# Kernel tuning notes

Hardware: AMD Instinct MI355X
Metric: run time of the kernel (lower is better)

Reference implementation:

```python
import jax, jax.numpy as jnp
import numpy as np


def setup_inputs() -> dict:
    key = jax.random.key(0)
    ks = jax.random.split(key, 7)
    B, C, N, F = 4, 8, 2048, 64
    H, O = 64, 64
    s_in = 1.0 / np.sqrt(F)
    s_h = 1.0 / np.sqrt(H)
    return {
        "x": jax.random.normal(ks[0], (B, C, N, F), dtype=jnp.float32),
        "W1": jax.random.uniform(ks[1], (H, F), jnp.float32, -s_in, s_in),
        "b1": jax.random.uniform(ks[2], (H,), jnp.float32, -s_in, s_in),
        "W2": jax.random.uniform(ks[3], (H, F), jnp.float32, -s_in, s_in),
        "b2": jax.random.uniform(ks[4], (H,), jnp.float32, -s_in, s_in),
        "W3": jax.random.uniform(ks[5], (O, F), jnp.float32, -s_in, s_in),
        "b3": jax.random.uniform(ks[6], (O,), jnp.float32, -s_in, s_in),
    }


def reference(x, W1, b1, W2, b2, W3, b3):
    # e1, e2: [B,C,N,H]  (torch Linear: x @ W^T + b)
    e1 = jnp.einsum("bcnf,hf->bcnh", x, W1) + b1
    e2 = jnp.einsum("bcnf,hf->bcnh", x, W2) + b2
    # adjacency via ReLU(e1 @ e2^T): [B,C,N,N]
    adj = jax.nn.relu(jnp.einsum("bcnh,bcmh->bcnm", e1, e2))
    # propagate: [B,C,N,F]
    h = jnp.einsum("bcnm,bcmf->bcnf", adj, x)
    # output projection (linear3): [B,C,N,O]
    return jnp.einsum("bcnf,of->bcno", h, W3) + b3
```

## Files before the change

### kernel.cpp

```cpp
#include <hip/hip_runtime.h>
#include <hip/hip_bf16.h>

#define BCH 32
#define NN  2048
#define DD  64

typedef __attribute__((ext_vector_type(8)))  __bf16 bf16x8;
typedef __attribute__((ext_vector_type(4)))  __bf16 bf16x4;
typedef __attribute__((ext_vector_type(4)))  float  f32x4;
typedef __attribute__((ext_vector_type(16))) float  f32x16;
typedef __attribute__((ext_vector_type(2)))  int    i32x2;
typedef __attribute__((ext_vector_type(4)))  int    i32x4;
typedef __attribute__((ext_vector_type(2)))  unsigned int u32x2;

__device__ inline f32x4 mfma16(bf16x8 a, bf16x8 b, f32x4 c) {
    return __builtin_amdgcn_mfma_f32_16x16x32_bf16(a, b, c, 0, 0, 0);
}
__device__ inline f32x16 mfma32(bf16x8 a, bf16x8 b, f32x16 c) {
    return __builtin_amdgcn_mfma_f32_32x32x16_bf16(a, b, c, 0, 0, 0);
}
__device__ inline void gload16(const void* g, void* l) {
    __builtin_amdgcn_global_load_lds(
        (const __attribute__((address_space(1))) void*)g,
        (__attribute__((address_space(3))) void*)l, 16, 0, 0);
}
__device__ inline void plswap(int& a, int& b) {
    u32x2 r = __builtin_amdgcn_permlane32_swap((unsigned)a, (unsigned)b, false, false);
    a = (int)r[0];
    b = (int)r[1];
}

__global__ __launch_bounds__(256) void prep_kernel(
    const float* __restrict__ x,
    const float* __restrict__ W1, const float* __restrict__ b1,
    const float* __restrict__ W2, const float* __restrict__ b2,
    const float* __restrict__ W3,
    __bf16* __restrict__ e1, __bf16* __restrict__ e2, __bf16* __restrict__ vT)
{
    const int t   = threadIdx.x;
    const int blk = blockIdx.x;
    const int bc  = blk >> 5, st = blk & 31;
    const long grow = (long)bc * NN + st * 64;
    const int w = t >> 6, l = t & 63, lg = l >> 4, li = l & 15;

    bf16x8 a[4][2];
    #pragma unroll
    for (int nb = 0; nb < 4; ++nb)
        #pragma unroll
        for (int kk = 0; kk < 2; ++kk) {
            const float* p = x + (grow + nb * 16 + li) * DD + kk * 32 + lg * 8;
            f32x4 v0 = *(const f32x4*)p, v1 = *(const f32x4*)(p + 4);
            #pragma unroll
            for (int j = 0; j < 4; ++j) {
                a[nb][kk][j]     = (__bf16)v0[j];
                a[nb][kk][4 + j] = (__bf16)v1[j];
            }
        }

    bf16x8 wf1[2], wf2[2], wf3[2];
    #pragma unroll
    for (int kk = 0; kk < 2; ++kk) {
        const float* p1 = W1 + (w * 16 + li) * DD + kk * 32 + lg * 8;
        const float* p2 = W2 + (w * 16 + li) * DD + kk * 32 + lg * 8;
        const float* p3 = W3 + (w * 16 + li) * DD + kk * 32 + lg * 8;
        f32x4 u0 = *(const f32x4*)p1, u1 = *(const f32x4*)(p1 + 4);
        f32x4 v0 = *(const f32x4*)p2, v1 = *(const f32x4*)(p2 + 4);
        f32x4 t0 = *(const f32x4*)p3, t1 = *(const f32x4*)(p3 + 4);
        #pragma unroll
        for (int j = 0; j < 4; ++j) {
            wf1[kk][j] = (__bf16)u0[j]; wf1[kk][4 + j] = (__bf16)u1[j];
            wf2[kk][j] = (__bf16)v0[j]; wf2[kk][4 + j] = (__bf16)v1[j];
            wf3[kk][j] = (__bf16)t0[j]; wf3[kk][4 + j] = (__bf16)t1[j];
        }
    }
    const f32x4 bq1 = *(const f32x4*)(b1 + w * 16 + lg * 4);
    const f32x4 bq2 = *(const f32x4*)(b2 + w * 16 + lg * 4);

    #pragma unroll
    for (int nb = 0; nb < 4; ++nb) {
        f32x4 acc1 = {0.f,0.f,0.f,0.f}, acc2 = {0.f,0.f,0.f,0.f}, acc3 = {0.f,0.f,0.f,0.f};
        #pragma unroll
        for (int kk = 0; kk < 2; ++kk) {
            acc1 = mfma16(wf1[kk], a[nb][kk], acc1);
            acc2 = mfma16(wf2[kk], a[nb][kk], acc2);
            acc3 = mfma16(a[nb][kk], wf3[kk], acc3);
        }
        bf16x4 q1, q2, q3;
        #pragma unroll
        for (int r = 0; r < 4; ++r) {
            q1[r] = (__bf16)(acc1[r] + bq1[r]);
            q2[r] = (__bf16)(acc2[r] + bq2[r]);
            q3[r] = (__bf16)acc3[r];
        }
        *(bf16x4*)&e1[(grow + nb * 16 + li) * DD + w * 16 + lg * 4] = q1;
        *(bf16x4*)&e2[(grow + nb * 16 + li) * DD + w * 16 + lg * 4] = q2;
        *(bf16x4*)&vT[((long)bc * DD + w * 16 + li) * NN + st * 64 + nb * 16 + lg * 4] = q3;
    }
}

__global__ __launch_bounds__(256, 4) void fused_kernel(
    const __bf16* __restrict__ e1, const __bf16* __restrict__ e2,
    const __bf16* __restrict__ vT, const float* __restrict__ b3,
    float* __restrict__ out)
{
    __shared__ __align__(16) unsigned char smem[32768];
    __bf16* e2t = (__bf16*)smem;
    __bf16* vTt = (__bf16*)(smem + 16384);
    float*  scratch = (float*)smem;

    const int t   = threadIdx.x;
    const int bid = blockIdx.x;
    const int x8 = bid & 7, jj = bid >> 3;
    const int bc = x8 * 4 + (jj >> 5), nt = jj & 31;

    const int w = t >> 6, l = t & 63;
    const int wn = w & 1, wm = w >> 1;
    const int l31 = l & 31, hi5 = l >> 5, l7 = l & 7, l3 = l >> 3;
    const int nbase = nt * 64 + wn * 32;

    bf16x8 e1f[4];
    {
        const __bf16* p = e1 + ((size_t)bc * NN + nbase + l31) * DD;
        #pragma unroll
        for (int kk = 0; kk < 4; ++kk)
            e1f[kk] = *(const bf16x8*)(p + kk * 16 + hi5 * 8);
    }

    f32x16 fz;
    #pragma unroll
    for (int i = 0; i < 16; ++i) fz[i] = 0.f;

    f32x16 hacc[2];
    #pragma unroll
    for (int fb = 0; fb < 2; ++fb)
        #pragma unroll
        for (int i = 0; i < 16; ++i) hacc[fb][i] = 0.f;

    const __bf16* e2h = e2 + (size_t)bc * NN * DD;
    const __bf16* vTh = vT + (size_t)bc * DD * NN;

    auto stage = [&](int buf, int kt) {
        #pragma unroll
        for (int ii = 0; ii < 2; ++ii) {
            const int ch  = w * 2 + ii;
            const int row = ch * 8 + l3;
            const int q   = l7 ^ l3;
            gload16(e2h + ((size_t)(kt * 64 + row)) * DD + q * 8, &e2t[buf * 4096 + ch * 512]);
            gload16(vTh + ((size_t)row) * NN + kt * 64 + q * 8, &vTt[buf * 4096 + ch * 512]);
        }
    };

    stage(0, 0);

    for (int kt = 0; kt < 32; ++kt) {
        const int buf = kt & 1;
        if (kt + 1 < 32) {
            stage(buf ^ 1, kt + 1);
            asm volatile("s_waitcnt vmcnt(4)" ::: "memory");
        } else {
            asm volatile("s_waitcnt vmcnt(0)" ::: "memory");
        }
        __builtin_amdgcn_sched_barrier(0);
        __builtin_amdgcn_s_barrier();

        f32x16 s;
        __builtin_amdgcn_s_setprio(1);
        {
            const int slot0 = ((hi5) ^ l7) * 8;
            bf16x8 ef0 = *(const bf16x8*)&e2t[buf * 4096 + (wm * 32 + l31) * 64 + slot0];
            s = mfma32(ef0, e1f[0], fz);
        }
        #pragma unroll
        for (int kk = 1; kk < 4; ++kk) {
            const int slot = ((kk * 2 + hi5) ^ l7) * 8;
            bf16x8 ef = *(const bf16x8*)&e2t[buf * 4096 + (wm * 32 + l31) * 64 + slot];
            s = mfma32(ef, e1f[kk], s);
        }
        __builtin_amdgcn_s_setprio(0);

        i32x2 Q[4];
        #pragma unroll
        for (int g = 0; g < 4; ++g) {
            bf16x4 q0;
            #pragma unroll
            for (int r = 0; r < 4; ++r) {
                float v = s[4 * g + r];
                q0[r] = (__bf16)(v > 0.f ? v : 0.f);
            }
            Q[g] = __builtin_bit_cast(i32x2, q0);
        }

        __builtin_amdgcn_s_setprio(1);
        #pragma unroll
        for (int kk2 = 0; kk2 < 2; ++kk2) {
            const int slot = ((wm * 4 + kk2 * 2 + hi5) ^ l7) * 8;
            bf16x8 vf0 = *(const bf16x8*)&vTt[buf * 4096 + (l31) * 64 + slot];
            bf16x8 vf1 = *(const bf16x8*)&vTt[buf * 4096 + (32 + l31) * 64 + slot];
            int a0 = Q[2 * kk2][0],     a1 = Q[2 * kk2][1];
            int b0 = Q[2 * kk2 + 1][0], b1 = Q[2 * kk2 + 1][1];
            plswap(a0, b0);
            plswap(a1, b1);
            i32x4 pfi = { a0, a1, b0, b1 };
            bf16x8 pf = __builtin_bit_cast(bf16x8, pfi);
            hacc[0] = mfma32(pf, vf0, hacc[0]);
            hacc[1] = mfma32(pf, vf1, hacc[1]);
        }
        __builtin_amdgcn_s_setprio(0);

        __builtin_amdgcn_s_barrier();
    }

    __syncthreads();
    if (wm == 1) {
        #pragma unroll
        for (int q = 0; q < 8; ++q) {
            f32x4 v;
            #pragma unroll
            for (int r = 0; r < 4; ++r) {
                const int idx = q * 4 + r;
                v[r] = hacc[idx >> 4][idx & 15];
            }
            *(f32x4*)&scratch[wn * 2048 + q * 256 + l * 4] = v;
        }
    }
    __syncthreads();
    if (wm == 0) {
        #pragma unroll
        for (int q = 0; q < 8; ++q) {
            f32x4 v = *(const f32x4*)&scratch[wn * 2048 + q * 256 + l * 4];
            #pragma unroll
            for (int r = 0; r < 4; ++r) {
                const int idx = q * 4 + r;
                hacc[idx >> 4][idx & 15] += v[r];
            }
        }
        const float bv0 = b3[l31], bv1 = b3[32 + l31];
        const size_t ob = ((size_t)bc * NN + nbase) * DD;
        #pragma unroll
        for (int reg = 0; reg < 16; ++reg) {
            const int n = (reg & 3) + 8 * (reg >> 2) + 4 * hi5;
            out[ob + (size_t)n * DD + l31]      = hacc[0][reg] + bv0;
            out[ob + (size_t)n * DD + 32 + l31] = hacc[1][reg] + bv1;
        }
    }
}

extern "C" void kernel_launch(void* const* d_in, const int* in_sizes, int n_in,
                              void* d_out, int out_size, void* d_ws, size_t ws_size,
                              hipStream_t stream) {
    const float* x  = (const float*)d_in[0];
    const float* W1 = (const float*)d_in[1];
    const float* b1 = (const float*)d_in[2];
    const float* W2 = (const float*)d_in[3];
    const float* b2 = (const float*)d_in[4];
    const float* W3 = (const float*)d_in[5];
    const float* b3 = (const float*)d_in[6];
    float* out = (float*)d_out;

    __bf16* e1 = (__bf16*)d_ws;
    __bf16* e2 = e1 + (size_t)BCH * NN * DD;
    __bf16* vT = e2 + (size_t)BCH * NN * DD;

    prep_kernel<<<dim3(1024), dim3(256), 0, stream>>>(x, W1, b1, W2, b2, W3, e1, e2, vT);
    fused_kernel<<<dim3(1024), dim3(256), 0, stream>>>(e1, e2, vT, b3, out);
}
```

Baseline: 69.43 us.

## Software-pipeline QK and PV stages across tiles; restructure prep kernel loops

The fused kernel's main loop becomes a two-stage software pipeline. The S=e2·e1 MFMAs for tile k+1 are interleaved with the PV MFMAs for tile k, using ping-pong Q and V-fragment registers, so the ReLU/pack step no longer serialises the MFMA chain. The prep kernel is reorganised so each wave owns 16 rows of x and loops over the output column blocks, which cuts the register-held x fragments but reloads the weights four times per wave. The extra register state for the double-buffered fragments may lower occupancy.

```diff
diff --git a/kernel.cpp b/kernel.cpp
--- a/kernel.cpp
+++ b/kernel.cpp
@@ -43,47 +43,42 @@
     const long grow = (long)bc * NN + st * 64;
     const int w = t >> 6, l = t & 63, lg = l >> 4, li = l & 15;
 
-    bf16x8 a[4][2];
-    #pragma unroll
-    for (int nb = 0; nb < 4; ++nb)
+    bf16x8 a[2];
+    #pragma unroll
+    for (int kk = 0; kk < 2; ++kk) {
+        const float* p = x + (grow + w * 16 + li) * DD + kk * 32 + lg * 8;
+        f32x4 v0 = *(const f32x4*)p, v1 = *(const f32x4*)(p + 4);
+        #pragma unroll
+        for (int j = 0; j < 4; ++j) { a[kk][j] = (__bf16)v0[j]; a[kk][4 + j] = (__bf16)v1[j]; }
+    }
+
+    #pragma unroll
+    for (int hb = 0; hb < 4; ++hb) {
+        bf16x8 wf1[2], wf2[2], wf3[2];
         #pragma unroll
         for (int kk = 0; kk < 2; ++kk) {
-            const float* p = x + (grow + nb * 16 + li) * DD + kk * 32 + lg * 8;
-            f32x4 v0 = *(const f32x4*)p, v1 = *(const f32x4*)(p + 4);
+            const float* p1 = W1 + (hb * 16 + li) * DD + kk * 32 + lg * 8;
+            const float* p2 = W2 + (hb * 16 + li) * DD + kk * 32 + lg * 8;
+            const float* p3 = W3 + (hb * 16 + li) * DD + kk * 32 + lg * 8;
+            f32x4 u0 = *(const f32x4*)p1, u1 = *(const f32x4*)(p1 + 4);
+            f32x4 v0 = *(const f32x4*)p2, v1 = *(const f32x4*)(p2 + 4);
+            f32x4 t0 = *(const f32x4*)p3, t1 = *(const f32x4*)(p3 + 4);
             #pragma unroll
             for (int j = 0; j < 4; ++j) {
-                a[nb][kk][j]     = (__bf16)v0[j];
-                a[nb][kk][4 + j] = (__bf16)v1[j];
-            }
-        }
-
-    bf16x8 wf1[2], wf2[2], wf3[2];
-    #pragma unroll
-    for (int kk = 0; kk < 2; ++kk) {
-        const float* p1 = W1 + (w * 16 + li) * DD + kk * 32 + lg * 8;
-        const float* p2 = W2 + (w * 16 + li) * DD + kk * 32 + lg * 8;
-        const float* p3 = W3 + (w * 16 + li) * DD + kk * 32 + lg * 8;
-        f32x4 u0 = *(const f32x4*)p1, u1 = *(const f32x4*)(p1 + 4);
-        f32x4 v0 = *(const f32x4*)p2, v1 = *(const f32x4*)(p2 + 4);
-        f32x4 t0 = *(const f32x4*)p3, t1 = *(const f32x4*)(p3 + 4);
-        #pragma unroll
-        for (int j = 0; j < 4; ++j) {
-            wf1[kk][j] = (__bf16)u0[j]; wf1[kk][4 + j] = (__bf16)u1[j];
-            wf2[kk][j] = (__bf16)v0[j]; wf2[kk][4 + j] = (__bf16)v1[j];
-            wf3[kk][j] = (__bf16)t0[j]; wf3[kk][4 + j] = (__bf16)t1[j];
-        }
-    }
-    const f32x4 bq1 = *(const f32x4*)(b1 + w * 16 + lg * 4);
-    const f32x4 bq2 = *(const f32x4*)(b2 + w * 16 + lg * 4);
-
-    #pragma unroll
-    for (int nb = 0; nb < 4; ++nb) {
+                wf1[kk][j] = (__bf16)u0[j]; wf1[kk][4 + j] = (__bf16)u1[j];
+                wf2[kk][j] = (__bf16)v0[j]; wf2[kk][4 + j] = (__bf16)v1[j];
+                wf3[kk][j] = (__bf16)t0[j]; wf3[kk][4 + j] = (__bf16)t1[j];
+            }
+        }
+        const f32x4 bq1 = *(const f32x4*)(b1 + hb * 16 + lg * 4);
+        const f32x4 bq2 = *(const f32x4*)(b2 + hb * 16 + lg * 4);
+
         f32x4 acc1 = {0.f,0.f,0.f,0.f}, acc2 = {0.f,0.f,0.f,0.f}, acc3 = {0.f,0.f,0.f,0.f};
         #pragma unroll
         for (int kk = 0; kk < 2; ++kk) {
-            acc1 = mfma16(wf1[kk], a[nb][kk], acc1);
-            acc2 = mfma16(wf2[kk], a[nb][kk], acc2);
-            acc3 = mfma16(a[nb][kk], wf3[kk], acc3);
+            acc1 = mfma16(wf1[kk], a[kk], acc1);
+            acc2 = mfma16(wf2[kk], a[kk], acc2);
+            acc3 = mfma16(a[kk], wf3[kk], acc3);
         }
         bf16x4 q1, q2, q3;
         #pragma unroll
@@ -92,9 +87,9 @@
             q2[r] = (__bf16)(acc2[r] + bq2[r]);
             q3[r] = (__bf16)acc3[r];
         }
-        *(bf16x4*)&e1[(grow + nb * 16 + li) * DD + w * 16 + lg * 4] = q1;
-        *(bf16x4*)&e2[(grow + nb * 16 + li) * DD + w * 16 + lg * 4] = q2;
-        *(bf16x4*)&vT[((long)bc * DD + w * 16 + li) * NN + st * 64 + nb * 16 + lg * 4] = q3;
+        *(bf16x4*)&e1[(grow + w * 16 + li) * DD + hb * 16 + lg * 4] = q1;
+        *(bf16x4*)&e2[(grow + w * 16 + li) * DD + hb * 16 + lg * 4] = q2;
+        *(bf16x4*)&vT[((long)bc * DD + hb * 16 + li) * NN + st * 64 + w * 16 + lg * 4] = q3;
     }
 }
 
@@ -104,9 +99,8 @@
     float* __restrict__ out)
 {
     __shared__ __align__(16) unsigned char smem[32768];
-    __bf16* e2t = (__bf16*)smem;
-    __bf16* vTt = (__bf16*)(smem + 16384);
-    float*  scratch = (float*)smem;
+    __bf16* lds = (__bf16*)smem;
+    float* scratch = (float*)smem;
 
     const int t   = threadIdx.x;
     const int bid = blockIdx.x;
@@ -118,6 +112,8 @@
     const int l31 = l & 31, hi5 = l >> 5, l7 = l & 7, l3 = l >> 3;
     const int nbase = nt * 64 + wn * 32;
 
+    const float bv0 = b3[l31], bv1 = b3[32 + l31];
+
     bf16x8 e1f[4];
     {
         const __bf16* p = e1 + ((size_t)bc * NN + nbase + l31) * DD;
@@ -129,7 +125,6 @@
     f32x16 fz;
     #pragma unroll
     for (int i = 0; i < 16; ++i) fz[i] = 0.f;
-
     f32x16 hacc[2];
     #pragma unroll
     for (int fb = 0; fb < 2; ++fb)
@@ -139,76 +134,108 @@
     const __bf16* e2h = e2 + (size_t)bc * NN * DD;
     const __bf16* vTh = vT + (size_t)bc * DD * NN;
 
-    auto stage = [&](int buf, int kt) {
+    auto stage = [&](int b, int kt) {
         #pragma unroll
         for (int ii = 0; ii < 2; ++ii) {
             const int ch  = w * 2 + ii;
             const int row = ch * 8 + l3;
             const int q   = l7 ^ l3;
-            gload16(e2h + ((size_t)(kt * 64 + row)) * DD + q * 8, &e2t[buf * 4096 + ch * 512]);
-            gload16(vTh + ((size_t)row) * NN + kt * 64 + q * 8, &vTt[buf * 4096 + ch * 512]);
-        }
-    };
-
-    stage(0, 0);
-
-    for (int kt = 0; kt < 32; ++kt) {
-        const int buf = kt & 1;
-        if (kt + 1 < 32) {
-            stage(buf ^ 1, kt + 1);
-            asm volatile("s_waitcnt vmcnt(4)" ::: "memory");
-        } else {
-            asm volatile("s_waitcnt vmcnt(0)" ::: "memory");
-        }
-        __builtin_amdgcn_sched_barrier(0);
-        __builtin_amdgcn_s_barrier();
-
-        f32x16 s;
-        __builtin_amdgcn_s_setprio(1);
-        {
-            const int slot0 = ((hi5) ^ l7) * 8;
-            bf16x8 ef0 = *(const bf16x8*)&e2t[buf * 4096 + (wm * 32 + l31) * 64 + slot0];
-            s = mfma32(ef0, e1f[0], fz);
-        }
+            gload16(e2h + ((size_t)(kt * 64 + row)) * DD + q * 8, &lds[b * 8192 + ch * 512]);
+            gload16(vTh + ((size_t)row) * NN + kt * 64 + q * 8, &lds[b * 8192 + 4096 + ch * 512]);
+        }
+    };
+    auto computeS = [&](int b, f32x16& sT) {
+        const int rowoff = b * 8192 + (wm * 32 + l31) * 64;
+        bf16x8 ef0 = *(const bf16x8*)&lds[rowoff + ((hi5) ^ l7) * 8];
+        sT = mfma32(ef0, e1f[0], fz);
         #pragma unroll
         for (int kk = 1; kk < 4; ++kk) {
-            const int slot = ((kk * 2 + hi5) ^ l7) * 8;
-            bf16x8 ef = *(const bf16x8*)&e2t[buf * 4096 + (wm * 32 + l31) * 64 + slot];
-            s = mfma32(ef, e1f[kk], s);
-        }
-        __builtin_amdgcn_s_setprio(0);
-
-        i32x2 Q[4];
+            bf16x8 ef = *(const bf16x8*)&lds[rowoff + ((kk * 2 + hi5) ^ l7) * 8];
+            sT = mfma32(ef, e1f[kk], sT);
+        }
+    };
+    auto loadVF = [&](int b, bf16x8 (&vf)[4]) {
+        #pragma unroll
+        for (int kk2 = 0; kk2 < 2; ++kk2) {
+            const int slot = ((wm * 4 + kk2 * 2 + hi5) ^ l7) * 8;
+            vf[kk2 * 2 + 0] = *(const bf16x8*)&lds[b * 8192 + 4096 + (l31) * 64 + slot];
+            vf[kk2 * 2 + 1] = *(const bf16x8*)&lds[b * 8192 + 4096 + (32 + l31) * 64 + slot];
+        }
+    };
+    auto packQ = [&](const f32x16& sT, i32x2 (&Q)[4]) {
         #pragma unroll
         for (int g = 0; g < 4; ++g) {
             bf16x4 q0;
             #pragma unroll
             for (int r = 0; r < 4; ++r) {
-                float v = s[4 * g + r];
+                float v = sT[4 * g + r];
                 q0[r] = (__bf16)(v > 0.f ? v : 0.f);
             }
             Q[g] = __builtin_bit_cast(i32x2, q0);
         }
-
-        __builtin_amdgcn_s_setprio(1);
+    };
+    auto doPV = [&](i32x2 (&Q)[4], bf16x8 (&vf)[4]) {
         #pragma unroll
         for (int kk2 = 0; kk2 < 2; ++kk2) {
-            const int slot = ((wm * 4 + kk2 * 2 + hi5) ^ l7) * 8;
-            bf16x8 vf0 = *(const bf16x8*)&vTt[buf * 4096 + (l31) * 64 + slot];
-            bf16x8 vf1 = *(const bf16x8*)&vTt[buf * 4096 + (32 + l31) * 64 + slot];
             int a0 = Q[2 * kk2][0],     a1 = Q[2 * kk2][1];
             int b0 = Q[2 * kk2 + 1][0], b1 = Q[2 * kk2 + 1][1];
             plswap(a0, b0);
             plswap(a1, b1);
             i32x4 pfi = { a0, a1, b0, b1 };
             bf16x8 pf = __builtin_bit_cast(bf16x8, pfi);
-            hacc[0] = mfma32(pf, vf0, hacc[0]);
-            hacc[1] = mfma32(pf, vf1, hacc[1]);
-        }
+            hacc[0] = mfma32(pf, vf[kk2 * 2 + 0], hacc[0]);
+            hacc[1] = mfma32(pf, vf[kk2 * 2 + 1], hacc[1]);
+        }
+    };
+
+    i32x2 Qa[4], Qb[4];
+    bf16x8 vfA[4], vfB[4];
+    f32x16 sT;
+
+    stage(0, 0);
+    stage(1, 1);
+    asm volatile("s_waitcnt vmcnt(4)" ::: "memory");
+    __builtin_amdgcn_sched_barrier(0);
+    __builtin_amdgcn_s_barrier();
+    computeS(0, sT);
+    loadVF(0, vfA);
+    packQ(sT, Qa);
+    __builtin_amdgcn_s_barrier();
+
+    for (int kt = 0; kt < 30; kt += 2) {
+        stage(0, kt + 2);
+        asm volatile("s_waitcnt vmcnt(4)" ::: "memory");
+        __builtin_amdgcn_sched_barrier(0);
+        __builtin_amdgcn_s_barrier();
+        __builtin_amdgcn_s_setprio(1);
+        computeS(1, sT);
+        loadVF(1, vfB);
+        doPV(Qa, vfA);
         __builtin_amdgcn_s_setprio(0);
-
-        __builtin_amdgcn_s_barrier();
-    }
+        packQ(sT, Qb);
+        __builtin_amdgcn_s_barrier();
+
+        stage(1, kt + 3);
+        asm volatile("s_waitcnt vmcnt(4)" ::: "memory");
+        __builtin_amdgcn_sched_barrier(0);
+        __builtin_amdgcn_s_barrier();
+        __builtin_amdgcn_s_setprio(1);
+        computeS(0, sT);
+        loadVF(0, vfA);
+        doPV(Qb, vfB);
+        __builtin_amdgcn_s_setprio(0);
+        packQ(sT, Qa);
+        __builtin_amdgcn_s_barrier();
+    }
+
+    asm volatile("s_waitcnt vmcnt(0)" ::: "memory");
+    __builtin_amdgcn_sched_barrier(0);
+    __builtin_amdgcn_s_barrier();
+    computeS(1, sT);
+    loadVF(1, vfB);
+    doPV(Qa, vfA);
+    packQ(sT, Qb);
+    doPV(Qb, vfB);
 
     __syncthreads();
     if (wm == 1) {
@@ -234,7 +261,6 @@
                 hacc[idx >> 4][idx & 15] += v[r];
             }
         }
-        const float bv0 = b3[l31], bv1 = b3[32 + l31];
         const size_t ob = ((size_t)bc * NN + nbase) * DD;
         #pragma unroll
         for (int reg = 0; reg < 16; ++reg) {
```

Measured after the change: 76.49 us. 10.2% more time.

## Pre-swizzle e2/vT into fragment layout and load MFMA operands directly from global

Applied to the files above, without the earlier changes.

The prep kernel now writes e2 and vT in a tiled, fragment-ordered layout, so each lane of the fused kernel can read its MFMA operands with direct 16-byte global loads. This removes LDS staging, the async global-to-LDS copies and the per-iteration block barriers. A register double buffer prefetches tile kt+1 while tile kt is computed. The cost is higher register pressure (occupancy hint lowered from 4 to 3), and each wave now reads operands from global/L2 that were previously shared through LDS across the waves of a block.

```diff
diff --git a/kernel.cpp b/kernel.cpp
--- a/kernel.cpp
+++ b/kernel.cpp
@@ -19,11 +19,6 @@
 __device__ inline f32x16 mfma32(bf16x8 a, bf16x8 b, f32x16 c) {
     return __builtin_amdgcn_mfma_f32_32x32x16_bf16(a, b, c, 0, 0, 0);
 }
-__device__ inline void gload16(const void* g, void* l) {
-    __builtin_amdgcn_global_load_lds(
-        (const __attribute__((address_space(1))) void*)g,
-        (__attribute__((address_space(3))) void*)l, 16, 0, 0);
-}
 __device__ inline void plswap(int& a, int& b) {
     u32x2 r = __builtin_amdgcn_permlane32_swap((unsigned)a, (unsigned)b, false, false);
     a = (int)r[0];
@@ -35,7 +30,7 @@
     const float* __restrict__ W1, const float* __restrict__ b1,
     const float* __restrict__ W2, const float* __restrict__ b2,
     const float* __restrict__ W3,
-    __bf16* __restrict__ e1, __bf16* __restrict__ e2, __bf16* __restrict__ vT)
+    __bf16* __restrict__ e1, __bf16* __restrict__ e2f, __bf16* __restrict__ vtf)
 {
     const int t   = threadIdx.x;
     const int blk = blockIdx.x;
@@ -76,6 +71,8 @@
     const f32x4 bq1 = *(const f32x4*)(b1 + w * 16 + lg * 4);
     const f32x4 bq2 = *(const f32x4*)(b2 + w * 16 + lg * 4);
 
+    const size_t ktbase = (size_t)(bc * 32 + st) * 4096;
+
     #pragma unroll
     for (int nb = 0; nb < 4; ++nb) {
         f32x4 acc1 = {0.f,0.f,0.f,0.f}, acc2 = {0.f,0.f,0.f,0.f}, acc3 = {0.f,0.f,0.f,0.f};
@@ -93,20 +90,17 @@
             q3[r] = (__bf16)acc3[r];
         }
         *(bf16x4*)&e1[(grow + nb * 16 + li) * DD + w * 16 + lg * 4] = q1;
-        *(bf16x4*)&e2[(grow + nb * 16 + li) * DD + w * 16 + lg * 4] = q2;
-        *(bf16x4*)&vT[((long)bc * DD + w * 16 + li) * NN + st * 64 + nb * 16 + lg * 4] = q3;
-    }
-}
-
-__global__ __launch_bounds__(256, 4) void fused_kernel(
-    const __bf16* __restrict__ e1, const __bf16* __restrict__ e2,
-    const __bf16* __restrict__ vT, const float* __restrict__ b3,
+        *(bf16x4*)&e2f[ktbase + (w * 2 + (lg >> 1)) * 512 + (nb * 16 + li) * 8 + (lg & 1) * 4] = q2;
+        *(bf16x4*)&vtf[ktbase + (nb * 2 + (lg >> 1)) * 512 + (w * 16 + li) * 8 + (lg & 1) * 4] = q3;
+    }
+}
+
+__global__ __launch_bounds__(256, 3) void fused_kernel(
+    const __bf16* __restrict__ e1, const __bf16* __restrict__ e2f,
+    const __bf16* __restrict__ vtf, const float* __restrict__ b3,
     float* __restrict__ out)
 {
-    __shared__ __align__(16) unsigned char smem[32768];
-    __bf16* e2t = (__bf16*)smem;
-    __bf16* vTt = (__bf16*)(smem + 16384);
-    float*  scratch = (float*)smem;
+    __shared__ float scratch[8192];
 
     const int t   = threadIdx.x;
     const int bid = blockIdx.x;
@@ -115,8 +109,10 @@
 
     const int w = t >> 6, l = t & 63;
     const int wn = w & 1, wm = w >> 1;
-    const int l31 = l & 31, hi5 = l >> 5, l7 = l & 7, l3 = l >> 3;
+    const int l31 = l & 31, hi5 = l >> 5;
     const int nbase = nt * 64 + wn * 32;
+
+    const float bv0 = b3[l31], bv1 = b3[32 + l31];
 
     bf16x8 e1f[4];
     {
@@ -129,88 +125,77 @@
     f32x16 fz;
     #pragma unroll
     for (int i = 0; i < 16; ++i) fz[i] = 0.f;
-
     f32x16 hacc[2];
     #pragma unroll
     for (int fb = 0; fb < 2; ++fb)
         #pragma unroll
         for (int i = 0; i < 16; ++i) hacc[fb][i] = 0.f;
 
-    const __bf16* e2h = e2 + (size_t)bc * NN * DD;
-    const __bf16* vTh = vT + (size_t)bc * DD * NN;
-
-    auto stage = [&](int buf, int kt) {
-        #pragma unroll
-        for (int ii = 0; ii < 2; ++ii) {
-            const int ch  = w * 2 + ii;
-            const int row = ch * 8 + l3;
-            const int q   = l7 ^ l3;
-            gload16(e2h + ((size_t)(kt * 64 + row)) * DD + q * 8, &e2t[buf * 4096 + ch * 512]);
-            gload16(vTh + ((size_t)row) * NN + kt * 64 + q * 8, &vTt[buf * 4096 + ch * 512]);
-        }
-    };
-
-    stage(0, 0);
-
-    for (int kt = 0; kt < 32; ++kt) {
-        const int buf = kt & 1;
-        if (kt + 1 < 32) {
-            stage(buf ^ 1, kt + 1);
-            asm volatile("s_waitcnt vmcnt(4)" ::: "memory");
-        } else {
-            asm volatile("s_waitcnt vmcnt(0)" ::: "memory");
-        }
-        __builtin_amdgcn_sched_barrier(0);
-        __builtin_amdgcn_s_barrier();
-
-        f32x16 s;
-        __builtin_amdgcn_s_setprio(1);
-        {
-            const int slot0 = ((hi5) ^ l7) * 8;
-            bf16x8 ef0 = *(const bf16x8*)&e2t[buf * 4096 + (wm * 32 + l31) * 64 + slot0];
-            s = mfma32(ef0, e1f[0], fz);
-        }
-        #pragma unroll
-        for (int kk = 1; kk < 4; ++kk) {
-            const int slot = ((kk * 2 + hi5) ^ l7) * 8;
-            bf16x8 ef = *(const bf16x8*)&e2t[buf * 4096 + (wm * 32 + l31) * 64 + slot];
-            s = mfma32(ef, e1f[kk], s);
-        }
-        __builtin_amdgcn_s_setprio(0);
-
-        i32x2 Q[4];
+    const __bf16* E2 = e2f + (size_t)bc * 131072 + hi5 * 512 + (wm * 32 + l31) * 8;
+    const __bf16* VT = vtf + (size_t)bc * 131072 + (wm * 4 + hi5) * 512 + l31 * 8;
+
+    auto loadEF = [&](int kt, bf16x8 (&ef)[4]) {
+        const __bf16* p = E2 + (size_t)kt * 4096;
+        #pragma unroll
+        for (int kk = 0; kk < 4; ++kk)
+            ef[kk] = *(const bf16x8*)(p + kk * 1024);
+    };
+    auto loadVF = [&](int kt, bf16x8 (&vf)[4]) {
+        const __bf16* p = VT + (size_t)kt * 4096;
+        #pragma unroll
+        for (int kk2 = 0; kk2 < 2; ++kk2) {
+            vf[kk2 * 2 + 0] = *(const bf16x8*)(p + kk2 * 1024);
+            vf[kk2 * 2 + 1] = *(const bf16x8*)(p + kk2 * 1024 + 256);
+        }
+    };
+    auto computeS = [&](bf16x8 (&ef)[4], f32x16& sT) {
+        sT = mfma32(ef[0], e1f[0], fz);
+        #pragma unroll
+        for (int kk = 1; kk < 4; ++kk)
+            sT = mfma32(ef[kk], e1f[kk], sT);
+    };
+    auto packQ = [&](const f32x16& sT, i32x2 (&Q)[4]) {
         #pragma unroll
         for (int g = 0; g < 4; ++g) {
             bf16x4 q0;
             #pragma unroll
             for (int r = 0; r < 4; ++r) {
-                float v = s[4 * g + r];
+                float v = sT[4 * g + r];
                 q0[r] = (__bf16)(v > 0.f ? v : 0.f);
             }
             Q[g] = __builtin_bit_cast(i32x2, q0);
         }
-
-        __builtin_amdgcn_s_setprio(1);
+    };
+    auto doPV = [&](i32x2 (&Q)[4], bf16x8 (&vf)[4]) {
         #pragma unroll
         for (int kk2 = 0; kk2 < 2; ++kk2) {
-            const int slot = ((wm * 4 + kk2 * 2 + hi5) ^ l7) * 8;
-            bf16x8 vf0 = *(const bf16x8*)&vTt[buf * 4096 + (l31) * 64 + slot];
-            bf16x8 vf1 = *(const bf16x8*)&vTt[buf * 4096 + (32 + l31) * 64 + slot];
             int a0 = Q[2 * kk2][0],     a1 = Q[2 * kk2][1];
             int b0 = Q[2 * kk2 + 1][0], b1 = Q[2 * kk2 + 1][1];
             plswap(a0, b0);
             plswap(a1, b1);
             i32x4 pfi = { a0, a1, b0, b1 };
             bf16x8 pf = __builtin_bit_cast(bf16x8, pfi);
-            hacc[0] = mfma32(pf, vf0, hacc[0]);
-            hacc[1] = mfma32(pf, vf1, hacc[1]);
-        }
-        __builtin_amdgcn_s_setprio(0);
-
-        __builtin_amdgcn_s_barrier();
-    }
-
-    __syncthreads();
+            hacc[0] = mfma32(pf, vf[kk2 * 2 + 0], hacc[0]);
+            hacc[1] = mfma32(pf, vf[kk2 * 2 + 1], hacc[1]);
+        }
+    };
+
+    bf16x8 efA[4], vfA[4], efB[4], vfB[4];
+    i32x2 Qa[4], Qb[4];
+    f32x16 sT;
+
+    loadEF(0, efA); loadVF(0, vfA);
+    for (int kt = 0; kt < 32; kt += 2) {
+        loadEF(kt + 1, efB); loadVF(kt + 1, vfB);
+        computeS(efA, sT);
+        packQ(sT, Qa);
+        doPV(Qa, vfA);
+        if (kt + 2 < 32) { loadEF(kt + 2, efA); loadVF(kt + 2, vfA); }
+        computeS(efB, sT);
+        packQ(sT, Qb);
+        doPV(Qb, vfB);
+    }
+
     if (wm == 1) {
         #pragma unroll
         for (int q = 0; q < 8; ++q) {
@@ -234,7 +219,6 @@
                 hacc[idx >> 4][idx & 15] += v[r];
             }
         }
-        const float bv0 = b3[l31], bv1 = b3[32 + l31];
         const size_t ob = ((size_t)bc * NN + nbase) * DD;
         #pragma unroll
         for (int reg = 0; reg < 16; ++reg) {
@@ -257,10 +241,10 @@
     const float* b3 = (const float*)d_in[6];
     float* out = (float*)d_out;
 
-    __bf16* e1 = (__bf16*)d_ws;
-    __bf16* e2 = e1 + (size_t)BCH * NN * DD;
-    __bf16* vT = e2 + (size_t)BCH * NN * DD;
-
-    prep_kernel<<<dim3(1024), dim3(256), 0, stream>>>(x, W1, b1, W2, b2, W3, e1, e2, vT);
-    fused_kernel<<<dim3(1024), dim3(256), 0, stream>>>(e1, e2, vT, b3, out);
-}
+    __bf16* e1  = (__bf16*)d_ws;
+    __bf16* e2f = e1 + (size_t)BCH * NN * DD;
+    __bf16* vtf = e2f + (size_t)BCH * NN * DD;
+
+    prep_kernel<<<dim3(1024), dim3(256), 0, stream>>>(x, W1, b1, W2, b2, W3, e1, e2f, vtf);
+    fused_kernel<<<dim3(1024), dim3(256), 0, stream>>>(e1, e2f, vtf, b3, out);
+}
```

New measurement: 67.12 us. 3.3% less time.
